# Performance work log

Hardware: AMD Instinct MI355X
Metric: run time of the kernel (lower is better)

## Reference

```python
import jax, jax.numpy as jnp
import numpy as np

B, NOTES, T, IN, H, NH = 32, 78, 128, 80, 128, 2  # batch, notes, time steps, input feats, time hidden, note hidden


def setup_inputs() -> dict:
    key = jax.random.key(0)
    ks = jax.random.split(key, 9)
    s = 0.1
    f32 = jnp.float32
    return {
        "x": jax.random.normal(ks[0], (B, NOTES, T, IN), f32),
        # time LSTM params (PyTorch layout: [4H, in], gate order i,f,g,o)
        "Wih_t": (jax.random.normal(ks[1], (4 * H, IN), f32) * s),
        "Whh_t": (jax.random.normal(ks[2], (4 * H, H), f32) * s),
        "bih_t": (jax.random.normal(ks[3], (4 * H,), f32) * s),
        "bhh_t": (jax.random.normal(ks[4], (4 * H,), f32) * s),
        # note LSTM params (hidden size 2)
        "Wih_n": (jax.random.normal(ks[5], (4 * NH, H), f32) * s),
        "Whh_n": (jax.random.normal(ks[6], (4 * NH, NH), f32) * s),
        "bih_n": (jax.random.normal(ks[7], (4 * NH,), f32) * s),
        "bhh_n": (jax.random.normal(ks[8], (4 * NH,), f32) * s),
    }


def _lstm(x, Wih, Whh, bih, bhh):
    # x: [N, L, in] -> all-step hidden states [N, L, H]; zero initial (h, c)
    N = x.shape[0]
    Hh = Whh.shape[1]
    b = bih + bhh

    def step(carry, xt):
        h, c = carry
        g = xt @ Wih.T + h @ Whh.T + b  # [N, 4H]
        i, f, gg, o = jnp.split(g, 4, axis=-1)
        c = jax.nn.sigmoid(f) * c + jax.nn.sigmoid(i) * jnp.tanh(gg)
        h = jax.nn.sigmoid(o) * jnp.tanh(c)
        return (h, c), h

    h0 = jnp.zeros((N, Hh), x.dtype)
    _, hs = jax.lax.scan(step, (h0, h0), x.transpose(1, 0, 2))  # hs: [L, N, H]
    return hs.transpose(1, 0, 2)


def reference(x, Wih_t, Whh_t, bih_t, bhh_t, Wih_n, Whh_n, bih_n, bhh_n):
    Bn = x.shape[0]
    # time LSTM: one sequence per (batch, note) -> batched into N = B*NOTES
    th = _lstm(x.reshape(Bn * NOTES, T, IN), Wih_t, Whh_t, bih_t, bhh_t)
    th = th.reshape(Bn, NOTES, T, H)
    # note LSTM: sequence over the 78-note axis at each time step -> batch B*T
    xn = th.transpose(0, 2, 1, 3).reshape(Bn * T, NOTES, H)
    nh = _lstm(xn, Wih_n, Whh_n, bih_n, bhh_n).reshape(Bn, T, NOTES, NH)
    return nh.reshape(Bn, T, NOTES * NH)  # [B, T, 156]
```

## Files before the change

### kernel.cpp

```cpp
#include <hip/hip_runtime.h>

#define B_     32
#define NOTES_ 78
#define T_     128
#define IN_    80
#define H_     128
#define NSEQ_  (B_*NOTES_)
#define MBLK   16
#define NBLK1  (NSEQ_/MBLK)
#define SEQ2_  (B_*T_)
#define XN8    (NSEQ_*T_*IN_/8)
#define SHSTR  136

typedef __attribute__((ext_vector_type(8))) short short8;
typedef __attribute__((ext_vector_type(4))) float f32x4;

__device__ __forceinline__ unsigned short f2bf(float f) {
    unsigned u; __builtin_memcpy(&u, &f, 4);
    u += 0x7fffu + ((u >> 16) & 1u);
    return (unsigned short)(u >> 16);
}
__device__ __forceinline__ short8 pack8(const float* p) {
    short8 r;
    #pragma unroll
    for (int k = 0; k < 8; ++k) r[k] = (short)f2bf(p[k]);
    return r;
}
__device__ __forceinline__ float rcpf(float x)  { return __builtin_amdgcn_rcpf(x); }
__device__ __forceinline__ float sigm(float x)  { return rcpf(1.f + __expf(-x)); }
__device__ __forceinline__ float tanh_(float x) { return 2.f * rcpf(1.f + __expf(-2.f*x)) - 1.f; }

__global__ __launch_bounds__(256) void xcvt_kernel(
    const float* __restrict__ x, unsigned short* __restrict__ xb)
{
    const int i = blockIdx.x * 256 + threadIdx.x;
    if (i < XN8) {
        const f32x4 a = *(const f32x4*)(x + (size_t)i * 8);
        const f32x4 b = *(const f32x4*)(x + (size_t)i * 8 + 4);
        short8 r;
        #pragma unroll
        for (int k = 0; k < 4; ++k) { r[k] = (short)f2bf(a[k]); r[4+k] = (short)f2bf(b[k]); }
        *(short8*)(xb + (size_t)i * 8) = r;
    }
}

#define ACCX_AND_PREFETCH                                                              \
    if (t + 1 < T_) {                                                                  \
        _Pragma("unroll")                                                              \
        for (int g = 0; g < 4; ++g) {                                                  \
            accX[g] = (f32x4){bg4[g], bg4[g], bg4[g], bg4[g]};                         \
            accX[g] = __builtin_amdgcn_mfma_f32_16x16x32_bf16(ax0, wf[g][0], accX[g], 0, 0, 0); \
            accX[g] = __builtin_amdgcn_mfma_f32_16x16x32_bf16(ax1, wf[g][1], accX[g], 0, 0, 0); \
            accX[g] = __builtin_amdgcn_mfma_f32_16x16x32_bf16(ax2, wf[g][2], accX[g], 0, 0, 0); \
        }                                                                              \
    }                                                                                  \
    if (t + 2 < T_) {                                                                  \
        if (XB16) {                                                                    \
            const unsigned short* p = xrb + (t + 2) * IN_;                             \
            ax0 = *(const short8*)(p + quad * 8);                                      \
            ax1 = *(const short8*)(p + 32 + quad * 8);                                 \
            if (quad < 2) ax2 = *(const short8*)(p + 64 + quad * 8);                   \
        } else {                                                                       \
            const float* p = xrf + (t + 2) * IN_;                                      \
            ax0 = pack8(p + quad * 8);                                                 \
            ax1 = pack8(p + 32 + quad * 8);                                            \
            if (quad < 2) ax2 = pack8(p + 64 + quad * 8);                              \
        }                                                                              \
    }

#define CELL_AND_H_WRITE                                                               \
    _Pragma("unroll")                                                                  \
    for (int r = 0; r < 4; ++r) {                                                      \
        const float cf = sigm(acc[1][r]) * cst[r] + sigm(acc[0][r]) * tanh_(acc[2][r]);\
        cst[r] = cf;                                                                   \
        const float h = sigm(acc[3][r]) * tanh_(cf);                                   \
        sHw[(quad * 4 + r) * SHSTR + j] = f2bf(h);                                     \
    }

#define GN_TILE                                                                        \
    if (t > 0 && wave == ((t - 1) & 7)) {                                              \
        f32x4 an = (f32x4){0.f, 0.f, 0.f, 0.f};                                        \
        _Pragma("unroll")                                                              \
        for (int kt = 0; kt < 4; ++kt)                                                 \
            an = __builtin_amdgcn_mfma_f32_16x16x32_bf16(ah[kt], wn[kt], an, 0, 0, 0); \
        if (m16 < 8) {                                                                 \
            _Pragma("unroll")                                                          \
            for (int r = 0; r < 4; ++r)                                                \
                Gn[gbase[r] + (unsigned)(t - 1) * (NOTES_ * 8)] = an[r] + bns;         \
        }                                                                              \
    }

template<bool XB16>
__global__ __launch_bounds__(512)
__attribute__((amdgpu_waves_per_eu(1, 2)))
void time_lstm_kernel(
    const void* __restrict__ xin,
    const float* __restrict__ Wih,
    const float* __restrict__ Whh,
    const float* __restrict__ bih,
    const float* __restrict__ bhh,
    const float* __restrict__ Wn,
    const float* __restrict__ bn1,
    const float* __restrict__ bn2,
    float* __restrict__ Gn)
{
    __shared__ unsigned short sH[2][MBLK * SHSTR];

    const int tid  = threadIdx.x;
    const int wave = tid >> 6, lane = tid & 63;
    const int m16  = lane & 15, quad = lane >> 4;
    const int seq0 = blockIdx.x * MBLK;
    const int j    = wave * 16 + m16;
    const bool grpB = (wave >= 4);

    for (int i = tid; i < 2 * MBLK * SHSTR; i += 512)
        ((unsigned short*)sH)[i] = 0;

    const short8 zero8 = (short8){0,0,0,0,0,0,0,0};
    short8 wf[4][3], hf[4][4];
    #pragma unroll
    for (int g = 0; g < 4; ++g) {
        const int n = g * H_ + j;
        #pragma unroll
        for (int kt = 0; kt < 3; ++kt) {
            const int k = kt * 32 + quad * 8;
            wf[g][kt] = (k < IN_) ? pack8(Wih + n * IN_ + k) : zero8;
        }
        #pragma unroll
        for (int kt = 0; kt < 4; ++kt)
            hf[g][kt] = pack8(Whh + n * H_ + kt * 32 + quad * 8);
    }

    short8 wn[4];
    #pragma unroll
    for (int kt = 0; kt < 4; ++kt)
        wn[kt] = (m16 < 8) ? pack8(Wn + m16 * H_ + kt * 32 + quad * 8) : zero8;
    const float bns = (m16 < 8) ? (bn1[m16] + bn2[m16]) : 0.f;
    unsigned gbase[4];
    #pragma unroll
    for (int r = 0; r < 4; ++r) {
        const int sq = seq0 + quad * 4 + r;
        const int bb = sq / NOTES_;
        const int nn = sq - bb * NOTES_;
        gbase[r] = ((unsigned)bb * (T_ * NOTES_) + (unsigned)nn) * 8u + (unsigned)m16;
    }

    float bg4[4];
    #pragma unroll
    for (int g = 0; g < 4; ++g) bg4[g] = bih[g * H_ + j] + bhh[g * H_ + j];

    const float* xrf = XB16 ? nullptr
        : ((const float*)xin + (size_t)(seq0 + m16) * T_ * IN_);
    const unsigned short* xrb = XB16
        ? ((const unsigned short*)xin + (size_t)(seq0 + m16) * T_ * IN_) : nullptr;

    short8 ax0, ax1, ax2 = zero8;
    if (XB16) {
        const unsigned short* p = xrb;
        ax0 = *(const short8*)(p + quad * 8);
        ax1 = *(const short8*)(p + 32 + quad * 8);
        if (quad < 2) ax2 = *(const short8*)(p + 64 + quad * 8);
    } else {
        const float* p = xrf;
        ax0 = pack8(p + quad * 8);
        ax1 = pack8(p + 32 + quad * 8);
        if (quad < 2) ax2 = pack8(p + 64 + quad * 8);
    }

    f32x4 accX[4];
    #pragma unroll
    for (int g = 0; g < 4; ++g) {
        accX[g] = (f32x4){bg4[g], bg4[g], bg4[g], bg4[g]};
        accX[g] = __builtin_amdgcn_mfma_f32_16x16x32_bf16(ax0, wf[g][0], accX[g], 0, 0, 0);
        accX[g] = __builtin_amdgcn_mfma_f32_16x16x32_bf16(ax1, wf[g][1], accX[g], 0, 0, 0);
        accX[g] = __builtin_amdgcn_mfma_f32_16x16x32_bf16(ax2, wf[g][2], accX[g], 0, 0, 0);
    }
    if (XB16) {
        const unsigned short* p = xrb + IN_;
        ax0 = *(const short8*)(p + quad * 8);
        ax1 = *(const short8*)(p + 32 + quad * 8);
        if (quad < 2) ax2 = *(const short8*)(p + 64 + quad * 8);
    } else {
        const float* p = xrf + IN_;
        ax0 = pack8(p + quad * 8);
        ax1 = pack8(p + 32 + quad * 8);
        if (quad < 2) ax2 = pack8(p + 64 + quad * 8);
    }

    float cst[4] = {0.f, 0.f, 0.f, 0.f};

    __syncthreads();

    for (int t = 0; t < T_; ++t) {
        const unsigned short* sHr = sH[t & 1];
        unsigned short*       sHw = sH[(t & 1) ^ 1];

        short8 ah[4];
        #pragma unroll
        for (int kt = 0; kt < 4; ++kt)
            ah[kt] = *(const short8*)(sHr + m16 * SHSTR + kt * 32 + quad * 8);

        f32x4 acc[4];
        #pragma unroll
        for (int g = 0; g < 4; ++g) {
            acc[g] = accX[g];
            #pragma unroll
            for (int kt = 0; kt < 4; ++kt)
                acc[g] = __builtin_amdgcn_mfma_f32_16x16x32_bf16(ah[kt], hf[g][kt], acc[g], 0, 0, 0);
        }

        if (grpB) {
            ACCX_AND_PREFETCH
            CELL_AND_H_WRITE
            GN_TILE
        } else {
            CELL_AND_H_WRITE
            GN_TILE
            ACCX_AND_PREFETCH
        }

        __builtin_amdgcn_sched_barrier(0);
        asm volatile("s_waitcnt lgkmcnt(0)" ::: "memory");
        __builtin_amdgcn_s_barrier();
        __builtin_amdgcn_sched_barrier(0);
    }

    if (wave == ((T_ - 1) & 7)) {
        const unsigned short* sHr = sH[T_ & 1];
        short8 ah[4];
        #pragma unroll
        for (int kt = 0; kt < 4; ++kt)
            ah[kt] = *(const short8*)(sHr + m16 * SHSTR + kt * 32 + quad * 8);
        f32x4 an = (f32x4){0.f, 0.f, 0.f, 0.f};
        #pragma unroll
        for (int kt = 0; kt < 4; ++kt)
            an = __builtin_amdgcn_mfma_f32_16x16x32_bf16(ah[kt], wn[kt], an, 0, 0, 0);
        if (m16 < 8) {
            #pragma unroll
            for (int r = 0; r < 4; ++r)
                Gn[gbase[r] + (unsigned)(T_ - 1) * (NOTES_ * 8)] = an[r] + bns;
        }
    }
}

__global__ __launch_bounds__(64) void note_out_kernel(
    const float* __restrict__ Gn,
    const float* __restrict__ Whh,
    float* __restrict__ out)
{
    const int q = blockIdx.x * 64 + threadIdx.x;
    if (q >= SEQ2_) return;

    float w0[8], w1[8];
    #pragma unroll
    for (int g = 0; g < 8; ++g) { w0[g] = Whh[g * 2]; w1[g] = Whh[g * 2 + 1]; }

    const float* gp = Gn + (size_t)q * (NOTES_ * 8);
    float* op = out + (size_t)q * (NOTES_ * 2);

    float h0 = 0.f, h1 = 0.f, c0 = 0.f, c1 = 0.f;
    f32x4 ga = *(const f32x4*)(gp);
    f32x4 gb = *(const f32x4*)(gp + 4);
    for (int n = 0; n < NOTES_; ++n) {
        f32x4 na, nb;
        if (n + 1 < NOTES_) {
            na = *(const f32x4*)(gp + (n + 1) * 8);
            nb = *(const f32x4*)(gp + (n + 1) * 8 + 4);
        }
        const float i0 = ga[0] + w0[0] * h0 + w1[0] * h1;
        const float i1 = ga[1] + w0[1] * h0 + w1[1] * h1;
        const float f0 = ga[2] + w0[2] * h0 + w1[2] * h1;
        const float f1 = ga[3] + w0[3] * h0 + w1[3] * h1;
        const float g0 = gb[0] + w0[4] * h0 + w1[4] * h1;
        const float g1 = gb[1] + w0[5] * h0 + w1[5] * h1;
        const float o0 = gb[2] + w0[6] * h0 + w1[6] * h1;
        const float o1 = gb[3] + w0[7] * h0 + w1[7] * h1;
        c0 = sigm(f0) * c0 + sigm(i0) * tanh_(g0);
        c1 = sigm(f1) * c1 + sigm(i1) * tanh_(g1);
        h0 = sigm(o0) * tanh_(c0);
        h1 = sigm(o1) * tanh_(c1);
        op[n * 2 + 0] = h0;
        op[n * 2 + 1] = h1;
        ga = na; gb = nb;
    }
}

extern "C" void kernel_launch(void* const* d_in, const int* in_sizes, int n_in,
                              void* d_out, int out_size, void* d_ws, size_t ws_size,
                              hipStream_t stream) {
    const float* x     = (const float*)d_in[0];
    const float* Wih_t = (const float*)d_in[1];
    const float* Whh_t = (const float*)d_in[2];
    const float* bih_t = (const float*)d_in[3];
    const float* bhh_t = (const float*)d_in[4];
    const float* Wih_n = (const float*)d_in[5];
    const float* Whh_n = (const float*)d_in[6];
    const float* bih_n = (const float*)d_in[7];
    const float* bhh_n = (const float*)d_in[8];
    float* out = (float*)d_out;

    const size_t xb_bytes = (size_t)NSEQ_ * T_ * IN_ * 2;
    const size_t gn_bytes = (size_t)SEQ2_ * NOTES_ * 8 * 4;

    if (ws_size >= xb_bytes + gn_bytes) {
        unsigned short* xb = (unsigned short*)d_ws;
        float* Gn = (float*)((char*)d_ws + xb_bytes);
        xcvt_kernel<<<(XN8 + 255) / 256, 256, 0, stream>>>(x, xb);
        time_lstm_kernel<true><<<NBLK1, 512, 0, stream>>>(
            xb, Wih_t, Whh_t, bih_t, bhh_t, Wih_n, bih_n, bhh_n, Gn);
        note_out_kernel<<<SEQ2_ / 64, 64, 0, stream>>>(Gn, Whh_n, out);
    } else {
        float* Gn = (float*)d_ws;
        time_lstm_kernel<false><<<NBLK1, 512, 0, stream>>>(
            x, Wih_t, Whh_t, bih_t, bhh_t, Wih_n, bih_n, bhh_n, Gn);
        note_out_kernel<<<SEQ2_ / 64, 64, 0, stream>>>(Gn, Whh_n, out);
    }
}
```

Baseline: 358.1 us.

## Split gate columns across 16 waves with LDS exchange of gate pre-activations

Doubles the time-LSTM block to 1024 threads. Each of two wave halves computes two of the four gates for the same hidden columns and swaps half its rows through shared memory, so every wave runs half the MFMAs and half the cell math per step. The aim is to shorten the serial per-step critical path of the recurrence. The cost is a second block barrier per step plus extra LDS traffic. It also moves the note-LSTM input weights into LDS to save registers, recomputes Gn addresses inline, merges the sigmoid and tanh reciprocals into a single rcp, and raises MFMA priority with s_setprio.

```diff
diff --git a/kernel.cpp b/kernel.cpp
--- a/kernel.cpp
+++ b/kernel.cpp
@@ -28,7 +28,7 @@
 }
 __device__ __forceinline__ float rcpf(float x)  { return __builtin_amdgcn_rcpf(x); }
 __device__ __forceinline__ float sigm(float x)  { return rcpf(1.f + __expf(-x)); }
-__device__ __forceinline__ float tanh_(float x) { return 2.f * rcpf(1.f + __expf(-2.f*x)) - 1.f; }
+__device__ __forceinline__ float tanhr(float x) { return 2.f * rcpf(1.f + __expf(-2.f*x)) - 1.f; }
 
 __global__ __launch_bounds__(256) void xcvt_kernel(
     const float* __restrict__ x, unsigned short* __restrict__ xb)
@@ -46,13 +46,15 @@
 
 #define ACCX_AND_PREFETCH                                                              \
     if (t + 1 < T_) {                                                                  \
+        __builtin_amdgcn_s_setprio(1);                                                 \
         _Pragma("unroll")                                                              \
-        for (int g = 0; g < 4; ++g) {                                                  \
-            accX[g] = (f32x4){bg4[g], bg4[g], bg4[g], bg4[g]};                         \
-            accX[g] = __builtin_amdgcn_mfma_f32_16x16x32_bf16(ax0, wf[g][0], accX[g], 0, 0, 0); \
-            accX[g] = __builtin_amdgcn_mfma_f32_16x16x32_bf16(ax1, wf[g][1], accX[g], 0, 0, 0); \
-            accX[g] = __builtin_amdgcn_mfma_f32_16x16x32_bf16(ax2, wf[g][2], accX[g], 0, 0, 0); \
+        for (int gl = 0; gl < 2; ++gl) {                                               \
+            accX[gl] = (f32x4){bg2[gl], bg2[gl], bg2[gl], bg2[gl]};                    \
+            accX[gl] = __builtin_amdgcn_mfma_f32_16x16x32_bf16(ax0, wf[gl][0], accX[gl], 0, 0, 0); \
+            accX[gl] = __builtin_amdgcn_mfma_f32_16x16x32_bf16(ax1, wf[gl][1], accX[gl], 0, 0, 0); \
+            accX[gl] = __builtin_amdgcn_mfma_f32_16x16x32_bf16(ax2, wf[gl][2], accX[gl], 0, 0, 0); \
         }                                                                              \
+        __builtin_amdgcn_s_setprio(0);                                                 \
     }                                                                                  \
     if (t + 2 < T_) {                                                                  \
         if (XB16) {                                                                    \
@@ -68,31 +70,30 @@
         }                                                                              \
     }
 
-#define CELL_AND_H_WRITE                                                               \
-    _Pragma("unroll")                                                                  \
-    for (int r = 0; r < 4; ++r) {                                                      \
-        const float cf = sigm(acc[1][r]) * cst[r] + sigm(acc[0][r]) * tanh_(acc[2][r]);\
-        cst[r] = cf;                                                                   \
-        const float h = sigm(acc[3][r]) * tanh_(cf);                                   \
-        sHw[(quad * 4 + r) * SHSTR + j] = f2bf(h);                                     \
-    }
-
-#define GN_TILE                                                                        \
-    if (t > 0 && wave == ((t - 1) & 7)) {                                              \
+#define GN_TILE(TM1)                                                                   \
+    if (wave == ((TM1) & 15)) {                                                        \
+        short8 wnk[4];                                                                 \
+        _Pragma("unroll")                                                              \
+        for (int kt = 0; kt < 4; ++kt)                                                 \
+            wnk[kt] = *(const short8*)(sWn + ((kt * 16 + m16) * 4 + quad) * 8);        \
         f32x4 an = (f32x4){0.f, 0.f, 0.f, 0.f};                                        \
         _Pragma("unroll")                                                              \
         for (int kt = 0; kt < 4; ++kt)                                                 \
-            an = __builtin_amdgcn_mfma_f32_16x16x32_bf16(ah[kt], wn[kt], an, 0, 0, 0); \
+            an = __builtin_amdgcn_mfma_f32_16x16x32_bf16(ah[kt], wnk[kt], an, 0, 0, 0);\
         if (m16 < 8) {                                                                 \
             _Pragma("unroll")                                                          \
-            for (int r = 0; r < 4; ++r)                                                \
-                Gn[gbase[r] + (unsigned)(t - 1) * (NOTES_ * 8)] = an[r] + bns;         \
+            for (int r = 0; r < 4; ++r) {                                              \
+                const int sq = seq0 + quad * 4 + r;                                    \
+                const int bb = sq / NOTES_;                                            \
+                const int nn = sq - bb * NOTES_;                                       \
+                Gn[((unsigned)bb * (T_ * NOTES_) + (unsigned)nn) * 8u + (unsigned)m16  \
+                   + (unsigned)(TM1) * (NOTES_ * 8)] = an[r] + bns;                    \
+            }                                                                          \
         }                                                                              \
     }
 
 template<bool XB16>
-__global__ __launch_bounds__(512)
-__attribute__((amdgpu_waves_per_eu(1, 2)))
+__global__ __launch_bounds__(1024)
 void time_lstm_kernel(
     const void* __restrict__ xin,
     const float* __restrict__ Wih,
@@ -105,49 +106,43 @@
     float* __restrict__ Gn)
 {
     __shared__ unsigned short sH[2][MBLK * SHSTR];
+    __shared__ float sX[8 * 2 * 64 * 4];
+    __shared__ unsigned short sWn[4 * 16 * 4 * 8];
 
     const int tid  = threadIdx.x;
     const int wave = tid >> 6, lane = tid & 63;
     const int m16  = lane & 15, quad = lane >> 4;
+    const int cg   = wave & 7, half = wave >> 3;
     const int seq0 = blockIdx.x * MBLK;
-    const int j    = wave * 16 + m16;
-    const bool grpB = (wave >= 4);
-
-    for (int i = tid; i < 2 * MBLK * SHSTR; i += 512)
+    const int j    = cg * 16 + m16;
+
+    for (int i = tid; i < 2 * MBLK * SHSTR; i += 1024)
         ((unsigned short*)sH)[i] = 0;
+    for (int i = tid; i < 4 * 16 * 4 * 8; i += 1024) {
+        const int e = i & 7, q = (i >> 3) & 3, m = (i >> 5) & 15, kt = i >> 9;
+        sWn[i] = (m < 8) ? f2bf(Wn[m * H_ + kt * 32 + q * 8 + e]) : (unsigned short)0;
+    }
 
     const short8 zero8 = (short8){0,0,0,0,0,0,0,0};
-    short8 wf[4][3], hf[4][4];
+    short8 wf[2][3], hf[2][4];
+    float  bg2[2];
     #pragma unroll
-    for (int g = 0; g < 4; ++g) {
-        const int n = g * H_ + j;
+    for (int gl = 0; gl < 2; ++gl) {
+        const int n = (half * 2 + gl) * H_ + j;
         #pragma unroll
         for (int kt = 0; kt < 3; ++kt) {
             const int k = kt * 32 + quad * 8;
-            wf[g][kt] = (k < IN_) ? pack8(Wih + n * IN_ + k) : zero8;
+            wf[gl][kt] = (k < IN_) ? pack8(Wih + n * IN_ + k) : zero8;
         }
         #pragma unroll
         for (int kt = 0; kt < 4; ++kt)
-            hf[g][kt] = pack8(Whh + n * H_ + kt * 32 + quad * 8);
-    }
-
-    short8 wn[4];
-    #pragma unroll
-    for (int kt = 0; kt < 4; ++kt)
-        wn[kt] = (m16 < 8) ? pack8(Wn + m16 * H_ + kt * 32 + quad * 8) : zero8;
+            hf[gl][kt] = pack8(Whh + n * H_ + kt * 32 + quad * 8);
+        bg2[gl] = bih[n] + bhh[n];
+    }
     const float bns = (m16 < 8) ? (bn1[m16] + bn2[m16]) : 0.f;
-    unsigned gbase[4];
-    #pragma unroll
-    for (int r = 0; r < 4; ++r) {
-        const int sq = seq0 + quad * 4 + r;
-        const int bb = sq / NOTES_;
-        const int nn = sq - bb * NOTES_;
-        gbase[r] = ((unsigned)bb * (T_ * NOTES_) + (unsigned)nn) * 8u + (unsigned)m16;
-    }
-
-    float bg4[4];
-    #pragma unroll
-    for (int g = 0; g < 4; ++g) bg4[g] = bih[g * H_ + j] + bhh[g * H_ + j];
+
+    const int xw_off = ((cg * 2 + half) * 64 + lane) * 4;
+    const int xr_off = ((cg * 2 + (half ^ 1)) * 64 + lane) * 4;
 
     const float* xrf = XB16 ? nullptr
         : ((const float*)xin + (size_t)(seq0 + m16) * T_ * IN_);
@@ -167,13 +162,13 @@
         if (quad < 2) ax2 = pack8(p + 64 + quad * 8);
     }
 
-    f32x4 accX[4];
+    f32x4 accX[2];
     #pragma unroll
-    for (int g = 0; g < 4; ++g) {
-        accX[g] = (f32x4){bg4[g], bg4[g], bg4[g], bg4[g]};
-        accX[g] = __builtin_amdgcn_mfma_f32_16x16x32_bf16(ax0, wf[g][0], accX[g], 0, 0, 0);
-        accX[g] = __builtin_amdgcn_mfma_f32_16x16x32_bf16(ax1, wf[g][1], accX[g], 0, 0, 0);
-        accX[g] = __builtin_amdgcn_mfma_f32_16x16x32_bf16(ax2, wf[g][2], accX[g], 0, 0, 0);
+    for (int gl = 0; gl < 2; ++gl) {
+        accX[gl] = (f32x4){bg2[gl], bg2[gl], bg2[gl], bg2[gl]};
+        accX[gl] = __builtin_amdgcn_mfma_f32_16x16x32_bf16(ax0, wf[gl][0], accX[gl], 0, 0, 0);
+        accX[gl] = __builtin_amdgcn_mfma_f32_16x16x32_bf16(ax1, wf[gl][1], accX[gl], 0, 0, 0);
+        accX[gl] = __builtin_amdgcn_mfma_f32_16x16x32_bf16(ax2, wf[gl][2], accX[gl], 0, 0, 0);
     }
     if (XB16) {
         const unsigned short* p = xrb + IN_;
@@ -187,7 +182,7 @@
         if (quad < 2) ax2 = pack8(p + 64 + quad * 8);
     }
 
-    float cst[4] = {0.f, 0.f, 0.f, 0.f};
+    float cst[2] = {0.f, 0.f};
 
     __syncthreads();
 
@@ -200,46 +195,90 @@
         for (int kt = 0; kt < 4; ++kt)
             ah[kt] = *(const short8*)(sHr + m16 * SHSTR + kt * 32 + quad * 8);
 
-        f32x4 acc[4];
-        #pragma unroll
-        for (int g = 0; g < 4; ++g) {
-            acc[g] = accX[g];
+        f32x4 acc[2];
+        __builtin_amdgcn_s_setprio(1);
+        #pragma unroll
+        for (int gl = 0; gl < 2; ++gl) {
+            acc[gl] = accX[gl];
             #pragma unroll
             for (int kt = 0; kt < 4; ++kt)
-                acc[g] = __builtin_amdgcn_mfma_f32_16x16x32_bf16(ah[kt], hf[g][kt], acc[g], 0, 0, 0);
-        }
-
-        if (grpB) {
+                acc[gl] = __builtin_amdgcn_mfma_f32_16x16x32_bf16(ah[kt], hf[gl][kt], acc[gl], 0, 0, 0);
+        }
+        __builtin_amdgcn_s_setprio(0);
+
+        f32x4 xw;
+        if (half == 0) xw = (f32x4){acc[0][2], acc[0][3], acc[1][2], acc[1][3]};
+        else           xw = (f32x4){acc[0][0], acc[0][1], acc[1][0], acc[1][1]};
+        *(f32x4*)(sX + xw_off) = xw;
+
+        if (half == 0) {
             ACCX_AND_PREFETCH
-            CELL_AND_H_WRITE
-            GN_TILE
-        } else {
-            CELL_AND_H_WRITE
-            GN_TILE
-            ACCX_AND_PREFETCH
+            if (t > 0) GN_TILE(t - 1)
         }
 
         __builtin_amdgcn_sched_barrier(0);
         asm volatile("s_waitcnt lgkmcnt(0)" ::: "memory");
         __builtin_amdgcn_s_barrier();
         __builtin_amdgcn_sched_barrier(0);
-    }
-
-    if (wave == ((T_ - 1) & 7)) {
+
+        const f32x4 rd = *(const f32x4*)(sX + xr_off);
+
+        float gi[2], gf[2], gg[2], go[2];
+        if (half == 0) {
+            gi[0] = acc[0][0]; gi[1] = acc[0][1];
+            gf[0] = acc[1][0]; gf[1] = acc[1][1];
+            gg[0] = rd[0];     gg[1] = rd[1];
+            go[0] = rd[2];     go[1] = rd[3];
+        } else {
+            gg[0] = acc[0][2]; gg[1] = acc[0][3];
+            go[0] = acc[1][2]; go[1] = acc[1][3];
+            gi[0] = rd[0];     gi[1] = rd[1];
+            gf[0] = rd[2];     gf[1] = rd[3];
+        }
+
+        float ei[2], ef[2], eg[2], eo[2];
+        #pragma unroll
+        for (int rr = 0; rr < 2; ++rr) {
+            ei[rr] = __expf(-gi[rr]);
+            ef[rr] = __expf(-gf[rr]);
+            eg[rr] = __expf(-2.f * gg[rr]);
+            eo[rr] = __expf(-go[rr]);
+        }
+        #pragma unroll
+        for (int rr = 0; rr < 2; ++rr) {
+            const float di = 1.f + ei[rr], df = 1.f + ef[rr];
+            const float dg = 1.f + eg[rr], dd = 1.f + eo[rr];
+            const float s1 = di * df, s2 = dg * dd;
+            const float R  = rcpf(s1 * s2);
+            const float Rs2 = R * s2, Rs1 = R * s1;
+            const float si = Rs2 * df;
+            const float sf = Rs2 * di;
+            const float so = Rs1 * dg;
+            const float tg = 2.f * (Rs1 * dd) - 1.f;
+            const float cf = sf * cst[rr] + si * tg;
+            cst[rr] = cf;
+            const float h = so * tanhr(cf);
+            sHw[(quad * 4 + half * 2 + rr) * SHSTR + j] = f2bf(h);
+        }
+
+        if (half == 1) {
+            ACCX_AND_PREFETCH
+            if (t > 0) GN_TILE(t - 1)
+        }
+
+        __builtin_amdgcn_sched_barrier(0);
+        asm volatile("s_waitcnt lgkmcnt(0)" ::: "memory");
+        __builtin_amdgcn_s_barrier();
+        __builtin_amdgcn_sched_barrier(0);
+    }
+
+    {
         const unsigned short* sHr = sH[T_ & 1];
         short8 ah[4];
         #pragma unroll
         for (int kt = 0; kt < 4; ++kt)
             ah[kt] = *(const short8*)(sHr + m16 * SHSTR + kt * 32 + quad * 8);
-        f32x4 an = (f32x4){0.f, 0.f, 0.f, 0.f};
-        #pragma unroll
-        for (int kt = 0; kt < 4; ++kt)
-            an = __builtin_amdgcn_mfma_f32_16x16x32_bf16(ah[kt], wn[kt], an, 0, 0, 0);
-        if (m16 < 8) {
-            #pragma unroll
-            for (int r = 0; r < 4; ++r)
-                Gn[gbase[r] + (unsigned)(T_ - 1) * (NOTES_ * 8)] = an[r] + bns;
-        }
+        GN_TILE(T_ - 1)
     }
 }
 
@@ -275,10 +314,10 @@
         const float g1 = gb[1] + w0[5] * h0 + w1[5] * h1;
         const float o0 = gb[2] + w0[6] * h0 + w1[6] * h1;
         const float o1 = gb[3] + w0[7] * h0 + w1[7] * h1;
-        c0 = sigm(f0) * c0 + sigm(i0) * tanh_(g0);
-        c1 = sigm(f1) * c1 + sigm(i1) * tanh_(g1);
-        h0 = sigm(o0) * tanh_(c0);
-        h1 = sigm(o1) * tanh_(c1);
+        c0 = sigm(f0) * c0 + sigm(i0) * tanhr(g0);
+        c1 = sigm(f1) * c1 + sigm(i1) * tanhr(g1);
+        h0 = sigm(o0) * tanhr(c0);
+        h1 = sigm(o1) * tanhr(c1);
         op[n * 2 + 0] = h0;
         op[n * 2 + 1] = h1;
         ga = na; gb = nb;
@@ -306,12 +345,12 @@
         unsigned short* xb = (unsigned short*)d_ws;
         float* Gn = (float*)((char*)d_ws + xb_bytes);
         xcvt_kernel<<<(XN8 + 255) / 256, 256, 0, stream>>>(x, xb);
-        time_lstm_kernel<true><<<NBLK1, 512, 0, stream>>>(
+        time_lstm_kernel<true><<<NBLK1, 1024, 0, stream>>>(
             xb, Wih_t, Whh_t, bih_t, bhh_t, Wih_n, bih_n, bhh_n, Gn);
         note_out_kernel<<<SEQ2_ / 64, 64, 0, stream>>>(Gn, Whh_n, out);
     } else {
         float* Gn = (float*)d_ws;
-        time_lstm_kernel<false><<<NBLK1, 512, 0, stream>>>(
+        time_lstm_kernel<false><<<NBLK1, 1024, 0, stream>>>(
             x, Wih_t, Whh_t, bih_t, bhh_t, Wih_n, bih_n, bhh_n, Gn);
         note_out_kernel<<<SEQ2_ / 64, 64, 0, stream>>>(Gn, Whh_n, out);
     }
```

Result: slower. 483.2 us (+34.9%).
